# Performance work log

Measured on AMD Instinct MI355X. Metric: run time of the kernel, lower is better.

Reference implementation:

```python
import jax, jax.numpy as jnp
import numpy as np


def setup_inputs() -> dict:
    key = jax.random.key(0)
    k1, k2, k3 = jax.random.split(key, 3)
    B, L, D = 8, 4096, 320
    CB_DIM, N_BOOKS = 16, 8192
    input_values = jax.random.normal(k1, (B, L, D), dtype=jnp.float32)
    # mask all ones -> static masked-select shape N = B*L
    mask_time_indices = jnp.ones((B, L), dtype=jnp.int32)
    # xavier_uniform for Linear(D -> CB_DIM, bias=False): limit = sqrt(6/(fan_in+fan_out))
    limit = float(np.sqrt(6.0 / (D + CB_DIM)))
    proj_weight = jax.random.uniform(k2, (CB_DIM, D), dtype=jnp.float32, minval=-limit, maxval=limit)
    code_book = jax.random.normal(k3, (N_BOOKS, CB_DIM), dtype=jnp.float32)
    return {"input_values": input_values, "mask_time_indices": mask_time_indices,
            "proj_weight": proj_weight, "code_book": code_book}


def reference(input_values, mask_time_indices, proj_weight, code_book):
    # input_values: [B, L, D]; mask is all-ones so masked select == flatten (static shape N=B*L)
    B, L, D = input_values.shape
    flat = input_values.reshape(B * L, D)  # [N, D]
    targets = flat @ proj_weight.T  # [N, cb_dim]  (random projection, no bias)
    # argmin over Euclidean norm == argmin over squared distance (monotone),
    # expanded form avoids the [N, n_books, cb_dim] broadcast intermediate.
    t2 = jnp.sum(targets * targets, axis=-1, keepdims=True)        # [N, 1]
    c2 = jnp.sum(code_book * code_book, axis=-1)                   # [n_books]
    d2 = t2 - 2.0 * (targets @ code_book.T) + c2                   # [N, n_books]
    labels = jnp.argmin(d2, axis=-1)                               # [N]
    return labels
```

## Files before the change

kernel.cpp:

```cpp
#include <hip/hip_runtime.h>

#define N_ROWS 32768
#define D_IN 320
#define CB 16
#define N_BOOKS 8192

typedef __attribute__((ext_vector_type(8))) short bf16x8;
typedef __attribute__((ext_vector_type(4))) float f32x4;
#define MFMA __builtin_amdgcn_mfma_f32_16x16x32_bf16
#define AS1 __attribute__((address_space(1)))
#define AS3 __attribute__((address_space(3)))

__device__ __forceinline__ unsigned short bf16rn(float f) {
  unsigned u = __float_as_uint(f);
  u += 0x7fffu + ((u >> 16) & 1u);
  return (unsigned short)(u >> 16);
}
__device__ __forceinline__ float bf16tof(unsigned short h) {
  return __uint_as_float(((unsigned)h) << 16);
}
__device__ __forceinline__ void gload_lds16(const short* g, short* l) {
  __builtin_amdgcn_global_load_lds((const AS1 unsigned int*)g, (AS3 unsigned int*)l, 16, 0, 0);
}

__global__ __launch_bounds__(256) void prep_kernel(const float* __restrict__ cbk,
                                                   short* __restrict__ bfrag,
                                                   float* __restrict__ nh_g) {
  const int j = blockIdx.x * 256 + threadIdx.x;
  const float4* src = (const float4*)(cbk + (size_t)j * CB);
  float4 a = src[0], b = src[1], c = src[2], d = src[3];
  float ce[16] = {a.x, a.y, a.z, a.w, b.x, b.y, b.z, b.w,
                  c.x, c.y, c.z, c.w, d.x, d.y, d.z, d.w};
  short c1[16], c2[16], c3[16];
  double s = 0.0;
#pragma unroll
  for (int i = 0; i < 16; i++) {
    s += (double)ce[i] * (double)ce[i];
    unsigned short x1 = bf16rn(ce[i]);
    float r1 = ce[i] - bf16tof(x1);
    unsigned short x2 = bf16rn(r1);
    float r2 = r1 - bf16tof(x2);
    unsigned short x3 = bf16rn(r2);
    c1[i] = (short)x1; c2[i] = (short)x2; c3[i] = (short)x3;
  }
  nh_g[j] = (float)(-0.5 * s);
  bf16x8 lo1, hi1, lo2, hi2, lo3, hi3;
#pragma unroll
  for (int i = 0; i < 8; i++) {
    lo1[i] = c1[i]; hi1[i] = c1[i + 8];
    lo2[i] = c2[i]; hi2[i] = c2[i + 8];
    lo3[i] = c3[i]; hi3[i] = c3[i + 8];
  }
  const int bt = j >> 4, n = j & 15;
  short* base = bfrag + (size_t)bt * 1536;
  *(bf16x8*)(base + 0 * 512 + (0 * 16 + n) * 8) = lo1;
  *(bf16x8*)(base + 0 * 512 + (1 * 16 + n) * 8) = hi1;
  *(bf16x8*)(base + 0 * 512 + (2 * 16 + n) * 8) = lo1;
  *(bf16x8*)(base + 0 * 512 + (3 * 16 + n) * 8) = hi1;
  *(bf16x8*)(base + 1 * 512 + (0 * 16 + n) * 8) = lo2;
  *(bf16x8*)(base + 1 * 512 + (1 * 16 + n) * 8) = hi2;
  *(bf16x8*)(base + 1 * 512 + (2 * 16 + n) * 8) = lo2;
  *(bf16x8*)(base + 1 * 512 + (3 * 16 + n) * 8) = hi2;
  *(bf16x8*)(base + 2 * 512 + (0 * 16 + n) * 8) = lo3;
  *(bf16x8*)(base + 2 * 512 + (1 * 16 + n) * 8) = hi3;
  *(bf16x8*)(base + 2 * 512 + (2 * 16 + n) * 8) = lo1;
  *(bf16x8*)(base + 2 * 512 + (3 * 16 + n) * 8) = hi1;
}

__global__ __launch_bounds__(256, 2) void proj_kernel(const float* __restrict__ x,
                                                      const float* __restrict__ w,
                                                      short* __restrict__ tsplit) {
  __shared__ __align__(16) short wfrag[3][10][64][8];
  __shared__ __align__(16) float xs[2][64 * 36];
  const int tid = threadIdx.x;
  const int lane = tid & 63;
  const int wv = tid >> 6;

  for (int i = tid; i < D_IN * CB; i += 256) {
    int d = i >> 4, o = i & 15;
    float f = w[o * D_IN + d];
    unsigned short h1 = bf16rn(f);
    float r1 = f - bf16tof(h1);
    unsigned short h2 = bf16rn(r1);
    float r2 = r1 - bf16tof(h2);
    unsigned short h3 = bf16rn(r2);
    int c = d >> 5, qq = (d >> 3) & 3, pos = d & 7;
    int ln = qq * 16 + o;
    wfrag[0][c][ln][pos] = (short)h1;
    wfrag[1][c][ln][pos] = (short)h2;
    wfrag[2][c][ln][pos] = (short)h3;
  }

  const float* xblk = x + (size_t)blockIdx.x * 64 * D_IN;
  {
    int row = tid >> 2, k0 = (tid & 3) * 8;
    float4 v0 = *(const float4*)(xblk + row * D_IN + k0);
    float4 v1 = *(const float4*)(xblk + row * D_IN + k0 + 4);
    *(float4*)&xs[0][row * 36 + k0] = v0;
    *(float4*)&xs[0][row * 36 + k0 + 4] = v1;
  }
  __syncthreads();

  const int m = lane & 15, q = lane >> 4;
  double dacc[4] = {0.0, 0.0, 0.0, 0.0};
  for (int c = 0; c < 10; c++) {
    const int buf = c & 1;
    if (c < 9) {
      int row = tid >> 2, k0 = (tid & 3) * 8;
      float4 v0 = *(const float4*)(xblk + row * D_IN + (c + 1) * 32 + k0);
      float4 v1 = *(const float4*)(xblk + row * D_IN + (c + 1) * 32 + k0 + 4);
      *(float4*)&xs[buf ^ 1][row * 36 + k0] = v0;
      *(float4*)&xs[buf ^ 1][row * 36 + k0 + 4] = v1;
    }
    const float* xp = &xs[buf][(wv * 16 + m) * 36 + q * 8];
    float4 xa = *(const float4*)xp;
    float4 xb = *(const float4*)(xp + 4);
    float xe[8] = {xa.x, xa.y, xa.z, xa.w, xb.x, xb.y, xb.z, xb.w};
    bf16x8 a1, a2, a3;
#pragma unroll
    for (int j = 0; j < 8; j++) {
      unsigned short h1 = bf16rn(xe[j]);
      float r1 = xe[j] - bf16tof(h1);
      unsigned short h2 = bf16rn(r1);
      float r2 = r1 - bf16tof(h2);
      unsigned short h3 = bf16rn(r2);
      a1[j] = (short)h1; a2[j] = (short)h2; a3[j] = (short)h3;
    }
    bf16x8 b1 = *(const bf16x8*)wfrag[0][c][lane];
    bf16x8 b2 = *(const bf16x8*)wfrag[1][c][lane];
    bf16x8 b3 = *(const bf16x8*)wfrag[2][c][lane];
    f32x4 g = {0.f, 0.f, 0.f, 0.f};
    g = MFMA(a1, b1, g, 0, 0, 0);
#pragma unroll
    for (int r = 0; r < 4; r++) dacc[r] += (double)g[r];
    g = (f32x4){0.f, 0.f, 0.f, 0.f};
    g = MFMA(a2, b1, g, 0, 0, 0);
    g = MFMA(a1, b2, g, 0, 0, 0);
#pragma unroll
    for (int r = 0; r < 4; r++) dacc[r] += (double)g[r];
    g = (f32x4){0.f, 0.f, 0.f, 0.f};
    g = MFMA(a3, b1, g, 0, 0, 0);
    g = MFMA(a1, b3, g, 0, 0, 0);
    g = MFMA(a2, b2, g, 0, 0, 0);
#pragma unroll
    for (int r = 0; r < 4; r++) dacc[r] += (double)g[r];
    __syncthreads();
  }

  float* tl = (float*)xs;
#pragma unroll
  for (int r = 0; r < 4; r++) tl[(wv * 16 + q * 4 + r) * 17 + m] = (float)dacc[r];
  __syncthreads();
  {
    int row_l = tid >> 2, p = tid & 3;
    short h1[4], h2[4], h3[4];
#pragma unroll
    for (int i = 0; i < 4; i++) {
      float f = tl[row_l * 17 + p * 4 + i];
      unsigned short a = bf16rn(f);
      float r1 = f - bf16tof(a);
      unsigned short b = bf16rn(r1);
      float r2 = r1 - bf16tof(b);
      unsigned short cc = bf16rn(r2);
      h1[i] = (short)a; h2[i] = (short)b; h3[i] = (short)cc;
    }
    size_t base = (size_t)(blockIdx.x * 64 + row_l) * 48;
    *(short4*)(tsplit + base + p * 4) = make_short4(h1[0], h1[1], h1[2], h1[3]);
    *(short4*)(tsplit + base + 16 + p * 4) = make_short4(h2[0], h2[1], h2[2], h2[3]);
    *(short4*)(tsplit + base + 32 + p * 4) = make_short4(h3[0], h3[1], h3[2], h3[3]);
  }
}

#define SC_H 8

__global__ __launch_bounds__(256, 2) void score_kernel(const short* __restrict__ tsplit,
                                                       const short* __restrict__ bfrag,
                                                       const float* __restrict__ nh_g,
                                                       float4* __restrict__ cand) {
  __shared__ __align__(16) short ldsb[2][6144];
  __shared__ float ldsnh[1024];
  const int tid = threadIdx.x;
  const int lane = tid & 63;
  const int wv = tid >> 6;
  const int m = lane & 15, q = lane >> 4;
  const int rb = blockIdx.x & 127;
  const int h = blockIdx.x >> 7;
  const int rowbase = rb * 256;

  bf16x8 A12[4], A13[4];
#pragma unroll
  for (int rt = 0; rt < 4; rt++) {
    int row = rowbase + wv * 64 + rt * 16 + m;
    const short* tp = tsplit + (size_t)row * 48;
    A12[rt] = *(const bf16x8*)(tp + q * 8);
    A13[rt] = *(const bf16x8*)(tp + q * 8 + ((q >= 2) ? 16 : 0));
  }
  for (int i = tid; i < 1024; i += 256) ldsnh[i] = nh_g[h * 1024 + i];

  const short* gq = bfrag + (size_t)h * 98304;
  {
    const short* g0 = gq + wv * 512 + lane * 8;
#pragma unroll
    for (int it = 0; it < 3; it++)
      gload_lds16(g0 + it * 2048, &ldsb[0][it * 2048 + wv * 512]);
  }

  float s1[4][4], s2[4][4];
  int i1[4][4];
#pragma unroll
  for (int rt = 0; rt < 4; rt++)
#pragma unroll
    for (int r = 0; r < 4; r++) { s1[rt][r] = -3.4e38f; s2[rt][r] = -3.4e38f; i1[rt][r] = 0; }

  __syncthreads();

  for (int sc = 0; sc < 16; sc++) {
    const int cur = sc & 1;
    if (sc < 15) {
      const short* gs = gq + (sc + 1) * 6144 + wv * 512 + lane * 8;
#pragma unroll
      for (int it = 0; it < 3; it++)
        gload_lds16(gs + it * 2048, &ldsb[cur ^ 1][it * 2048 + wv * 512]);
    }
#pragma unroll
    for (int bt = 0; bt < 4; bt++) {
      const short* bp = &ldsb[cur][bt * 1536];
      bf16x8 b1 = *(const bf16x8*)(bp + 0 * 512 + lane * 8);
      bf16x8 b2 = *(const bf16x8*)(bp + 1 * 512 + lane * 8);
      bf16x8 b3 = *(const bf16x8*)(bp + 2 * 512 + lane * 8);
      const int btg = sc * 4 + bt;
      float nh0 = ldsnh[btg * 16 + m];
      f32x4 ci = {nh0, nh0, nh0, nh0};
      const int colv = h * 1024 + btg * 16 + m;
#pragma unroll
      for (int rt = 0; rt < 4; rt++) {
        f32x4 acc = MFMA(A12[rt], b1, ci, 0, 0, 0);
        acc = MFMA(A12[rt], b2, acc, 0, 0, 0);
        acc = MFMA(A13[rt], b3, acc, 0, 0, 0);
#pragma unroll
        for (int r = 0; r < 4; r++) {
          float v = acc[r];
          float s1o = s1[rt][r];
          s2[rt][r] = __builtin_amdgcn_fmed3f(v, s1o, s2[rt][r]);
          s1[rt][r] = fmaxf(s1o, v);
          i1[rt][r] = (v > s1o) ? colv : i1[rt][r];
        }
      }
    }
    __syncthreads();
  }

#pragma unroll
  for (int rt = 0; rt < 4; rt++)
#pragma unroll
    for (int r = 0; r < 4; r++) {
      float a1v = s1[rt][r], a2v = s2[rt][r];
      int ai = i1[rt][r];
#pragma unroll
      for (int msk = 1; msk <= 8; msk <<= 1) {
        float o1 = __shfl_xor(a1v, msk);
        float o2 = __shfl_xor(a2v, msk);
        int oi = __shfl_xor(ai, msk);
        if (o1 > a1v) {
          a2v = fmaxf(a1v, o2); a1v = o1; ai = oi;
        } else {
          a2v = fmaxf(a2v, o1);
          if (o1 == a1v && oi < ai) ai = oi;
        }
      }
      if (m == 0) {
        int row = rowbase + wv * 64 + rt * 16 + q * 4 + r;
        cand[(size_t)h * N_ROWS + row] = make_float4(a1v, a2v, __int_as_float(ai), 0.f);
      }
    }
}

#define MARGIN_EPS 1.0e-4f

__global__ __launch_bounds__(256) void reduce_fb_kernel(const float4* __restrict__ cand,
                                                        const float* __restrict__ x,
                                                        const float* __restrict__ w,
                                                        const float* __restrict__ codebook,
                                                        int* __restrict__ out) {
  __shared__ int flagged[256];
  __shared__ double ps[16][17];
  __shared__ double tsh[16];
  __shared__ double rs[256];
  __shared__ int ri[256];
  const int tid = threadIdx.x;
  const int base = blockIdx.x * 256;
  {
    const int r = base + tid;
    float S1 = -3.4e38f, S2 = -3.4e38f;
    int I = 0;
#pragma unroll
    for (int h = 0; h < SC_H; h++) {
      float4 v = cand[(size_t)h * N_ROWS + r];
      if (v.x > S1) {
        S2 = fmaxf(S1, v.y); S1 = v.x; I = __float_as_int(v.z);
      } else {
        S2 = fmaxf(S2, v.x);
      }
    }
    out[r] = I;
    flagged[tid] = (S1 - S2 < MARGIN_EPS) ? 1 : 0;
  }
  __syncthreads();

  for (int rr = 0; rr < 256; rr++) {
    if (!flagged[rr]) continue;
    const int row = base + rr;
    {
      int o = tid & 15, c = tid >> 4;
      double p = 0.0;
      for (int k = 0; k < 20; k++) {
        int d = c * 20 + k;
        p = fma((double)x[(size_t)row * D_IN + d], (double)w[o * D_IN + d], p);
      }
      ps[c][o] = p;
    }
    __syncthreads();
    if (tid < 16) {
      double t = 0.0;
      for (int c = 0; c < 16; c++) t += ps[c][tid];
      tsh[tid] = t;
    }
    __syncthreads();
    double t[16];
#pragma unroll
    for (int i = 0; i < 16; i++) t[i] = tsh[i];
    double bs = -1.0e300;
    int bi = 0;
    for (int j = tid; j < N_BOOKS; j += 256) {
      const float* cp = codebook + (size_t)j * CB;
      double dot = 0.0, cc = 0.0;
#pragma unroll
      for (int i = 0; i < 16; i++) {
        double cv = (double)cp[i];
        dot = fma(t[i], cv, dot);
        cc = fma(cv, cv, cc);
      }
      double mv = dot - 0.5 * cc;
      if (mv > bs) { bs = mv; bi = j; }
    }
    rs[tid] = bs; ri[tid] = bi;
    __syncthreads();
    for (int s = 128; s > 0; s >>= 1) {
      if (tid < s) {
        double os = rs[tid + s]; int oi = ri[tid + s];
        if (os > rs[tid] || (os == rs[tid] && oi < ri[tid])) { rs[tid] = os; ri[tid] = oi; }
      }
      __syncthreads();
    }
    if (tid == 0) out[row] = ri[0];
    __syncthreads();
  }
}

extern "C" void kernel_launch(void* const* d_in, const int* in_sizes, int n_in,
                              void* d_out, int out_size, void* d_ws, size_t ws_size,
                              hipStream_t stream) {
  (void)in_sizes; (void)n_in; (void)out_size; (void)ws_size;
  const float* x = (const float*)d_in[0];
  const float* w = (const float*)d_in[2];
  const float* codebook = (const float*)d_in[3];

  char* ws = (char*)d_ws;
  short* tsplit = (short*)(ws);
  short* bfrag = (short*)(ws + (3 << 20));
  float* nh_g = (float*)(ws + 4718592);
  float4* cand = (float4*)(ws + (5 << 20));
  int* out = (int*)d_out;

  prep_kernel<<<N_BOOKS / 256, 256, 0, stream>>>(codebook, bfrag, nh_g);
  proj_kernel<<<N_ROWS / 64, 256, 0, stream>>>(x, w, tsplit);
  score_kernel<<<128 * SC_H, 256, 0, stream>>>(tsplit, bfrag, nh_g, cand);
  reduce_fb_kernel<<<N_ROWS / 256, 256, 0, stream>>>(cand, x, w, codebook, out);
}
```

Measured before the change: 206.6 us.

## Stream codebook fragments from global into registers instead of LDS double buffering

```diff
diff --git a/kernel.cpp b/kernel.cpp
--- a/kernel.cpp
+++ b/kernel.cpp
@@ -8,8 +8,6 @@
 typedef __attribute__((ext_vector_type(8))) short bf16x8;
 typedef __attribute__((ext_vector_type(4))) float f32x4;
 #define MFMA __builtin_amdgcn_mfma_f32_16x16x32_bf16
-#define AS1 __attribute__((address_space(1)))
-#define AS3 __attribute__((address_space(3)))
 
 __device__ __forceinline__ unsigned short bf16rn(float f) {
   unsigned u = __float_as_uint(f);
@@ -18,9 +16,6 @@
 }
 __device__ __forceinline__ float bf16tof(unsigned short h) {
   return __uint_as_float(((unsigned)h) << 16);
-}
-__device__ __forceinline__ void gload_lds16(const short* g, short* l) {
-  __builtin_amdgcn_global_load_lds((const AS1 unsigned int*)g, (AS3 unsigned int*)l, 16, 0, 0);
 }
 
 __global__ __launch_bounds__(256) void prep_kernel(const float* __restrict__ cbk,
@@ -173,12 +168,12 @@
 
 #define SC_H 8
 
-__global__ __launch_bounds__(256, 2) void score_kernel(const short* __restrict__ tsplit,
-                                                       const short* __restrict__ bfrag,
-                                                       const float* __restrict__ nh_g,
-                                                       float4* __restrict__ cand) {
-  __shared__ __align__(16) short ldsb[2][6144];
-  __shared__ float ldsnh[1024];
+__global__ __attribute__((amdgpu_flat_work_group_size(256, 256)))
+__attribute__((amdgpu_waves_per_eu(2, 4)))
+void score_kernel(const short* __restrict__ tsplit,
+                  const short* __restrict__ bfrag,
+                  const float* __restrict__ nh_g,
+                  float4* __restrict__ cand) {
   const int tid = threadIdx.x;
   const int lane = tid & 63;
   const int wv = tid >> 6;
@@ -195,15 +190,6 @@
     A12[rt] = *(const bf16x8*)(tp + q * 8);
     A13[rt] = *(const bf16x8*)(tp + q * 8 + ((q >= 2) ? 16 : 0));
   }
-  for (int i = tid; i < 1024; i += 256) ldsnh[i] = nh_g[h * 1024 + i];
-
-  const short* gq = bfrag + (size_t)h * 98304;
-  {
-    const short* g0 = gq + wv * 512 + lane * 8;
-#pragma unroll
-    for (int it = 0; it < 3; it++)
-      gload_lds16(g0 + it * 2048, &ldsb[0][it * 2048 + wv * 512]);
-  }
 
   float s1[4][4], s2[4][4];
   int i1[4][4];
@@ -212,42 +198,38 @@
 #pragma unroll
     for (int r = 0; r < 4; r++) { s1[rt][r] = -3.4e38f; s2[rt][r] = -3.4e38f; i1[rt][r] = 0; }
 
-  __syncthreads();
-
-  for (int sc = 0; sc < 16; sc++) {
-    const int cur = sc & 1;
-    if (sc < 15) {
-      const short* gs = gq + (sc + 1) * 6144 + wv * 512 + lane * 8;
-#pragma unroll
-      for (int it = 0; it < 3; it++)
-        gload_lds16(gs + it * 2048, &ldsb[cur ^ 1][it * 2048 + wv * 512]);
-    }
-#pragma unroll
-    for (int bt = 0; bt < 4; bt++) {
-      const short* bp = &ldsb[cur][bt * 1536];
-      bf16x8 b1 = *(const bf16x8*)(bp + 0 * 512 + lane * 8);
-      bf16x8 b2 = *(const bf16x8*)(bp + 1 * 512 + lane * 8);
-      bf16x8 b3 = *(const bf16x8*)(bp + 2 * 512 + lane * 8);
-      const int btg = sc * 4 + bt;
-      float nh0 = ldsnh[btg * 16 + m];
-      f32x4 ci = {nh0, nh0, nh0, nh0};
-      const int colv = h * 1024 + btg * 16 + m;
-#pragma unroll
-      for (int rt = 0; rt < 4; rt++) {
-        f32x4 acc = MFMA(A12[rt], b1, ci, 0, 0, 0);
-        acc = MFMA(A12[rt], b2, acc, 0, 0, 0);
-        acc = MFMA(A13[rt], b3, acc, 0, 0, 0);
-#pragma unroll
-        for (int r = 0; r < 4; r++) {
-          float v = acc[r];
-          float s1o = s1[rt][r];
-          s2[rt][r] = __builtin_amdgcn_fmed3f(v, s1o, s2[rt][r]);
-          s1[rt][r] = fmaxf(s1o, v);
-          i1[rt][r] = (v > s1o) ? colv : i1[rt][r];
-        }
-      }
-    }
-    __syncthreads();
+  const short* gq = bfrag + (size_t)h * 98304 + lane * 8;
+  const float* nhp = nh_g + h * 1024 + m;
+
+  bf16x8 b1 = *(const bf16x8*)(gq);
+  bf16x8 b2 = *(const bf16x8*)(gq + 512);
+  bf16x8 b3 = *(const bf16x8*)(gq + 1024);
+  float nh0 = nhp[0];
+
+  for (int bt = 0; bt < 64; bt++) {
+    const short* bp = gq + (bt + 1) * 1536;
+    bf16x8 n1 = *(const bf16x8*)(bp);
+    bf16x8 n2 = *(const bf16x8*)(bp + 512);
+    bf16x8 n3 = *(const bf16x8*)(bp + 1024);
+    float nn = nhp[(bt + 1) * 16];
+
+    f32x4 ci = {nh0, nh0, nh0, nh0};
+    const int colv = h * 1024 + bt * 16 + m;
+#pragma unroll
+    for (int rt = 0; rt < 4; rt++) {
+      f32x4 acc = MFMA(A12[rt], b1, ci, 0, 0, 0);
+      acc = MFMA(A12[rt], b2, acc, 0, 0, 0);
+      acc = MFMA(A13[rt], b3, acc, 0, 0, 0);
+#pragma unroll
+      for (int r = 0; r < 4; r++) {
+        float v = acc[r];
+        float s1o = s1[rt][r];
+        s2[rt][r] = __builtin_amdgcn_fmed3f(v, s1o, s2[rt][r]);
+        s1[rt][r] = fmaxf(s1o, v);
+        i1[rt][r] = (v > s1o) ? colv : i1[rt][r];
+      }
+    }
+    b1 = n1; b2 = n2; b3 = n3; nh0 = nn;
   }
 
 #pragma unroll
```

After: 210.9 us. 1.02x slower.

## Drop third bf16 split term in scoring and compact fallback rows into worklist

Applied to the files above, without the earlier changes.

```diff
diff --git a/kernel.cpp b/kernel.cpp
--- a/kernel.cpp
+++ b/kernel.cpp
@@ -25,13 +25,15 @@
 
 __global__ __launch_bounds__(256) void prep_kernel(const float* __restrict__ cbk,
                                                    short* __restrict__ bfrag,
-                                                   float* __restrict__ nh_g) {
+                                                   float* __restrict__ nh_g,
+                                                   int* __restrict__ ctr) {
+  if (blockIdx.x == 0 && threadIdx.x == 0) *ctr = 0;
   const int j = blockIdx.x * 256 + threadIdx.x;
   const float4* src = (const float4*)(cbk + (size_t)j * CB);
   float4 a = src[0], b = src[1], c = src[2], d = src[3];
   float ce[16] = {a.x, a.y, a.z, a.w, b.x, b.y, b.z, b.w,
                   c.x, c.y, c.z, c.w, d.x, d.y, d.z, d.w};
-  short c1[16], c2[16], c3[16];
+  short c1[16], c2[16];
   double s = 0.0;
 #pragma unroll
   for (int i = 0; i < 16; i++) {
@@ -39,32 +41,25 @@
     unsigned short x1 = bf16rn(ce[i]);
     float r1 = ce[i] - bf16tof(x1);
     unsigned short x2 = bf16rn(r1);
-    float r2 = r1 - bf16tof(x2);
-    unsigned short x3 = bf16rn(r2);
-    c1[i] = (short)x1; c2[i] = (short)x2; c3[i] = (short)x3;
+    c1[i] = (short)x1; c2[i] = (short)x2;
   }
   nh_g[j] = (float)(-0.5 * s);
-  bf16x8 lo1, hi1, lo2, hi2, lo3, hi3;
+  bf16x8 lo1, hi1, lo2, hi2;
 #pragma unroll
   for (int i = 0; i < 8; i++) {
     lo1[i] = c1[i]; hi1[i] = c1[i + 8];
     lo2[i] = c2[i]; hi2[i] = c2[i + 8];
-    lo3[i] = c3[i]; hi3[i] = c3[i + 8];
   }
   const int bt = j >> 4, n = j & 15;
-  short* base = bfrag + (size_t)bt * 1536;
-  *(bf16x8*)(base + 0 * 512 + (0 * 16 + n) * 8) = lo1;
-  *(bf16x8*)(base + 0 * 512 + (1 * 16 + n) * 8) = hi1;
-  *(bf16x8*)(base + 0 * 512 + (2 * 16 + n) * 8) = lo1;
-  *(bf16x8*)(base + 0 * 512 + (3 * 16 + n) * 8) = hi1;
-  *(bf16x8*)(base + 1 * 512 + (0 * 16 + n) * 8) = lo2;
-  *(bf16x8*)(base + 1 * 512 + (1 * 16 + n) * 8) = hi2;
-  *(bf16x8*)(base + 1 * 512 + (2 * 16 + n) * 8) = lo2;
-  *(bf16x8*)(base + 1 * 512 + (3 * 16 + n) * 8) = hi2;
-  *(bf16x8*)(base + 2 * 512 + (0 * 16 + n) * 8) = lo3;
-  *(bf16x8*)(base + 2 * 512 + (1 * 16 + n) * 8) = hi3;
-  *(bf16x8*)(base + 2 * 512 + (2 * 16 + n) * 8) = lo1;
-  *(bf16x8*)(base + 2 * 512 + (3 * 16 + n) * 8) = hi1;
+  short* base = bfrag + (size_t)bt * 1024;
+  *(bf16x8*)(base + (0 * 16 + n) * 8) = lo1;
+  *(bf16x8*)(base + (1 * 16 + n) * 8) = hi1;
+  *(bf16x8*)(base + (2 * 16 + n) * 8) = lo1;
+  *(bf16x8*)(base + (3 * 16 + n) * 8) = hi1;
+  *(bf16x8*)(base + 512 + (0 * 16 + n) * 8) = lo2;
+  *(bf16x8*)(base + 512 + (1 * 16 + n) * 8) = hi2;
+  *(bf16x8*)(base + 512 + (2 * 16 + n) * 8) = lo2;
+  *(bf16x8*)(base + 512 + (3 * 16 + n) * 8) = hi2;
 }
 
 __global__ __launch_bounds__(256, 2) void proj_kernel(const float* __restrict__ x,
@@ -177,7 +172,7 @@
                                                        const short* __restrict__ bfrag,
                                                        const float* __restrict__ nh_g,
                                                        float4* __restrict__ cand) {
-  __shared__ __align__(16) short ldsb[2][6144];
+  __shared__ __align__(16) short ldsb[2][8192];
   __shared__ float ldsnh[1024];
   const int tid = threadIdx.x;
   const int lane = tid & 63;
@@ -187,21 +182,19 @@
   const int h = blockIdx.x >> 7;
   const int rowbase = rb * 256;
 
-  bf16x8 A12[4], A13[4];
+  bf16x8 A12[4];
 #pragma unroll
   for (int rt = 0; rt < 4; rt++) {
     int row = rowbase + wv * 64 + rt * 16 + m;
-    const short* tp = tsplit + (size_t)row * 48;
-    A12[rt] = *(const bf16x8*)(tp + q * 8);
-    A13[rt] = *(const bf16x8*)(tp + q * 8 + ((q >= 2) ? 16 : 0));
+    A12[rt] = *(const bf16x8*)(tsplit + (size_t)row * 48 + q * 8);
   }
   for (int i = tid; i < 1024; i += 256) ldsnh[i] = nh_g[h * 1024 + i];
 
-  const short* gq = bfrag + (size_t)h * 98304;
+  const short* gq = bfrag + (size_t)h * 65536;
   {
     const short* g0 = gq + wv * 512 + lane * 8;
 #pragma unroll
-    for (int it = 0; it < 3; it++)
+    for (int it = 0; it < 4; it++)
       gload_lds16(g0 + it * 2048, &ldsb[0][it * 2048 + wv * 512]);
   }
 
@@ -214,21 +207,20 @@
 
   __syncthreads();
 
-  for (int sc = 0; sc < 16; sc++) {
+  for (int sc = 0; sc < 8; sc++) {
     const int cur = sc & 1;
-    if (sc < 15) {
-      const short* gs = gq + (sc + 1) * 6144 + wv * 512 + lane * 8;
-#pragma unroll
-      for (int it = 0; it < 3; it++)
+    if (sc < 7) {
+      const short* gs = gq + (sc + 1) * 8192 + wv * 512 + lane * 8;
+#pragma unroll
+      for (int it = 0; it < 4; it++)
         gload_lds16(gs + it * 2048, &ldsb[cur ^ 1][it * 2048 + wv * 512]);
     }
 #pragma unroll
-    for (int bt = 0; bt < 4; bt++) {
-      const short* bp = &ldsb[cur][bt * 1536];
-      bf16x8 b1 = *(const bf16x8*)(bp + 0 * 512 + lane * 8);
-      bf16x8 b2 = *(const bf16x8*)(bp + 1 * 512 + lane * 8);
-      bf16x8 b3 = *(const bf16x8*)(bp + 2 * 512 + lane * 8);
-      const int btg = sc * 4 + bt;
+    for (int bt = 0; bt < 8; bt++) {
+      const short* bp = &ldsb[cur][bt * 1024];
+      bf16x8 b1 = *(const bf16x8*)(bp + lane * 8);
+      bf16x8 b2 = *(const bf16x8*)(bp + 512 + lane * 8);
+      const int btg = sc * 8 + bt;
       float nh0 = ldsnh[btg * 16 + m];
       f32x4 ci = {nh0, nh0, nh0, nh0};
       const int colv = h * 1024 + btg * 16 + m;
@@ -236,7 +228,6 @@
       for (int rt = 0; rt < 4; rt++) {
         f32x4 acc = MFMA(A12[rt], b1, ci, 0, 0, 0);
         acc = MFMA(A12[rt], b2, acc, 0, 0, 0);
-        acc = MFMA(A13[rt], b3, acc, 0, 0, 0);
 #pragma unroll
         for (int r = 0; r < 4; r++) {
           float v = acc[r];
@@ -275,41 +266,46 @@
     }
 }
 
-#define MARGIN_EPS 1.0e-4f
-
-__global__ __launch_bounds__(256) void reduce_fb_kernel(const float4* __restrict__ cand,
-                                                        const float* __restrict__ x,
-                                                        const float* __restrict__ w,
-                                                        const float* __restrict__ codebook,
-                                                        int* __restrict__ out) {
-  __shared__ int flagged[256];
+#define MARGIN_EPS 1.0e-3f
+
+__global__ __launch_bounds__(256) void merge_flag_kernel(const float4* __restrict__ cand,
+                                                         int* __restrict__ out,
+                                                         int* __restrict__ list,
+                                                         int* __restrict__ ctr) {
+  const int r = blockIdx.x * 256 + threadIdx.x;
+  float S1 = -3.4e38f, S2 = -3.4e38f;
+  int I = 0;
+#pragma unroll
+  for (int h = 0; h < SC_H; h++) {
+    float4 v = cand[(size_t)h * N_ROWS + r];
+    if (v.x > S1) {
+      S2 = fmaxf(S1, v.y); S1 = v.x; I = __float_as_int(v.z);
+    } else {
+      S2 = fmaxf(S2, v.x);
+    }
+  }
+  out[r] = I;
+  if (S1 - S2 < MARGIN_EPS) {
+    int slot = atomicAdd(ctr, 1);
+    list[slot] = r;
+  }
+}
+
+__global__ __launch_bounds__(256) void rescore_kernel(const int* __restrict__ list,
+                                                      const int* __restrict__ ctr,
+                                                      const float* __restrict__ x,
+                                                      const float* __restrict__ w,
+                                                      const float* __restrict__ codebook,
+                                                      int* __restrict__ out) {
   __shared__ double ps[16][17];
   __shared__ double tsh[16];
   __shared__ double rs[256];
   __shared__ int ri[256];
   const int tid = threadIdx.x;
-  const int base = blockIdx.x * 256;
-  {
-    const int r = base + tid;
-    float S1 = -3.4e38f, S2 = -3.4e38f;
-    int I = 0;
-#pragma unroll
-    for (int h = 0; h < SC_H; h++) {
-      float4 v = cand[(size_t)h * N_ROWS + r];
-      if (v.x > S1) {
-        S2 = fmaxf(S1, v.y); S1 = v.x; I = __float_as_int(v.z);
-      } else {
-        S2 = fmaxf(S2, v.x);
-      }
-    }
-    out[r] = I;
-    flagged[tid] = (S1 - S2 < MARGIN_EPS) ? 1 : 0;
-  }
-  __syncthreads();
-
-  for (int rr = 0; rr < 256; rr++) {
-    if (!flagged[rr]) continue;
-    const int row = base + rr;
+  const int total = ctr[0];
+
+  for (int it = blockIdx.x; it < total; it += gridDim.x) {
+    const int row = list[it];
     {
       int o = tid & 15, c = tid >> 4;
       double p = 0.0;
@@ -368,12 +364,15 @@
   char* ws = (char*)d_ws;
   short* tsplit = (short*)(ws);
   short* bfrag = (short*)(ws + (3 << 20));
-  float* nh_g = (float*)(ws + 4718592);
+  float* nh_g = (float*)(ws + (4 << 20));
+  int* list = (int*)(ws + 4231168);
+  int* ctr = (int*)(ws + 4362240);
   float4* cand = (float4*)(ws + (5 << 20));
   int* out = (int*)d_out;
 
-  prep_kernel<<<N_BOOKS / 256, 256, 0, stream>>>(codebook, bfrag, nh_g);
+  prep_kernel<<<N_BOOKS / 256, 256, 0, stream>>>(codebook, bfrag, nh_g, ctr);
   proj_kernel<<<N_ROWS / 64, 256, 0, stream>>>(x, w, tsplit);
   score_kernel<<<128 * SC_H, 256, 0, stream>>>(tsplit, bfrag, nh_g, cand);
-  reduce_fb_kernel<<<N_ROWS / 256, 256, 0, stream>>>(cand, x, w, codebook, out);
-}
+  merge_flag_kernel<<<N_ROWS / 256, 256, 0, stream>>>(cand, out, list, ctr);
+  rescore_kernel<<<512, 256, 0, stream>>>(list, ctr, x, w, codebook, out);
+}
```

After: 182.3 us. 1.13x faster.
